# Kernel optimization log

Measured on AMD Instinct MI355X. Metric: run time of the kernel, lower is better.

## Reference

```python
import jax, jax.numpy as jnp
import numpy as np

T, B, H = 512, 256, 256


def setup_inputs() -> dict:
    key = jax.random.key(0)
    k1, k2, k3, k4 = jax.random.split(key, 4)
    ins = jax.random.normal(k1, (T, B, H), jnp.float32)
    resets = jax.random.randint(k2, (T, B), 0, 2) > 0  # bool reset mask
    carry = jnp.zeros((B, H), jnp.float32)
    scale = 1.0 / np.sqrt(H).astype(np.float32)
    # Fused GRU weights: columns ordered [r | z | n] for input and hidden projections.
    Wi = jax.random.normal(k3, (H, 3 * H), jnp.float32) * scale  # dense_i kernels (ir, iz, in)
    Wh = jax.random.normal(k4, (H, 3 * H), jnp.float32) * scale  # dense_h kernels (hr, hz, hn)
    bi = jnp.zeros((3 * H,), jnp.float32)   # dense_i biases (ir, iz, in)
    bhn = jnp.zeros((H,), jnp.float32)      # dense_h bias, only the 'hn' gate has one in flax GRUCell
    return dict(ins=ins, resets=resets, carry=carry, Wi=Wi, bi=bi, Wh=Wh, bhn=bhn)


def reference(ins, resets, carry, Wi, bi, Wh, bhn):
    """Faithful jax version of ScannedRNN: per-step reset-masked flax GRUCell scan.

    flax GRUCell math:
      r = sigmoid(x@Wir + bir + h@Whr)
      z = sigmoid(x@Wiz + biz + h@Whz)
      n = tanh(x@Win + bin + r * (h@Whn + bhn))
      h' = (1-z)*n + z*h ; output y = h'
    Reset mask zeroes the carry before the cell (initialize_carry -> zeros).
    """
    def step(h, xt):
        x, reset = xt  # x: [B,H], reset: [B]
        h = jnp.where(reset[:, None], jnp.zeros_like(h), h)
        gi = x @ Wi + bi          # [B, 3H]
        gh = h @ Wh               # [B, 3H]
        ir_, iz_, in_ = jnp.split(gi, 3, axis=-1)
        hr_, hz_, hn_ = jnp.split(gh, 3, axis=-1)
        r = jax.nn.sigmoid(ir_ + hr_)
        z = jax.nn.sigmoid(iz_ + hz_)
        n = jnp.tanh(in_ + r * (hn_ + bhn))
        h_new = (1.0 - z) * n + z * h
        return h_new, h_new

    _, ys = jax.lax.scan(step, carry, (ins, resets))
    return ys  # [T, B, H]
```

## Files before the change

kernel.cpp:

```cpp
#include <hip/hip_runtime.h>
#include <stdint.h>


typedef __attribute__((ext_vector_type(8))) __bf16 bf16x8;
typedef __attribute__((ext_vector_type(4))) float f32x4;

__device__ __forceinline__ float bf2f(unsigned short u) {
    union { unsigned int i; float f; } v; v.i = ((unsigned int)u) << 16; return v.f;
}
__device__ __forceinline__ unsigned short f2bf(float f) {
    union { float f; unsigned int i; } v; v.f = f;
    unsigned int x = v.i;
    x = x + 0x7fffu + ((x >> 16) & 1u);
    return (unsigned short)(x >> 16);
}
__device__ __forceinline__ float fsig(float x) {
    return __builtin_amdgcn_rcpf(1.f + __builtin_amdgcn_exp2f(-1.442695041f * x));
}
__device__ __forceinline__ float ftanh(float x) {
    return 1.f - 2.f * __builtin_amdgcn_rcpf(1.f + __builtin_amdgcn_exp2f(2.885390082f * x));
}

__global__ void prep_weights(const float* __restrict__ Wi, const float* __restrict__ Wh,
                             unsigned short* __restrict__ WiT, unsigned short* __restrict__ WhT) {
    const int idx = blockIdx.x * 256 + threadIdx.x;
    const float* src = blockIdx.y ? Wh : Wi;
    unsigned short* dst = blockIdx.y ? WhT : WiT;
    const int c = idx >> 8, k = idx & 255;
    dst[c * 256 + k] = f2bf(src[k * 768 + c]);
}

__launch_bounds__(512, 2)
__global__ void gi_gemm(const float* __restrict__ ins, const unsigned short* __restrict__ WiT,
                        const float* __restrict__ bi, unsigned int* __restrict__ GI32) {
    __shared__ unsigned short a_buf[2][16 * 264];

    const int tid = threadIdx.x;
    const int lane = tid & 63, wv = tid >> 6;
    const int quad = lane >> 4, n16 = lane & 15;

    bf16x8 wfrag[3][2][8];
#pragma unroll
    for (int g = 0; g < 3; ++g)
#pragma unroll
        for (int tl = 0; tl < 2; ++tl) {
            const int c = g * 256 + wv * 32 + tl * 16 + n16;
            const unsigned short* src = WiT + c * 256 + quad * 8;
#pragma unroll
            for (int kt = 0; kt < 8; ++kt)
                wfrag[g][tl][kt] = *(const bf16x8*)(src + kt * 32);
        }
    float bi_r[3][2];
#pragma unroll
    for (int g = 0; g < 3; ++g)
#pragma unroll
        for (int tl = 0; tl < 2; ++tl)
            bi_r[g][tl] = bi[g * 256 + wv * 32 + tl * 16 + n16];

    const int srow = tid >> 5;
    const int scol = (tid & 31) * 8;

    float4 p0, p1;
    {
        const float* p = ins + (size_t)blockIdx.x * 16 * 256 + tid * 8;
        p0 = *(const float4*)p; p1 = *(const float4*)(p + 4);
    }

    int buf = 0;
    for (int i = 0; i < 32; ++i) {
        const int chunk = blockIdx.x + i * 256;
        {
            bf16x8 av;
            av[0] = (__bf16)p0.x; av[1] = (__bf16)p0.y; av[2] = (__bf16)p0.z; av[3] = (__bf16)p0.w;
            av[4] = (__bf16)p1.x; av[5] = (__bf16)p1.y; av[6] = (__bf16)p1.z; av[7] = (__bf16)p1.w;
            *(bf16x8*)(&a_buf[buf][srow * 264 + scol]) = av;
        }
        if (i + 1 < 32) {
            const float* p = ins + (size_t)(blockIdx.x + (i + 1) * 256) * 16 * 256 + tid * 8;
            p0 = *(const float4*)p; p1 = *(const float4*)(p + 4);
        }
        __syncthreads();

        f32x4 acc[3][2] = {};
#pragma unroll
        for (int kt = 0; kt < 8; ++kt) {
            bf16x8 af = *(const bf16x8*)(&a_buf[buf][n16 * 264 + kt * 32 + quad * 8]);
#pragma unroll
            for (int g = 0; g < 3; ++g)
#pragma unroll
                for (int tl = 0; tl < 2; ++tl)
                    acc[g][tl] = __builtin_amdgcn_mfma_f32_16x16x32_bf16(af, wfrag[g][tl][kt], acc[g][tl], 0, 0, 0);
        }
        {
            const int t = chunk >> 4;
            const int b0 = (chunk & 15) * 16;
#pragma unroll
            for (int g = 0; g < 3; ++g)
#pragma unroll
                for (int r = 0; r < 4; ++r) {
                    const unsigned int lo = f2bf(acc[g][0][r] + bi_r[g][0]);
                    const unsigned int hi = f2bf(acc[g][1][r] + bi_r[g][1]);
                    GI32[((size_t)t * 256 + b0 + quad * 4 + r) * 384 + g * 128 + wv * 16 + n16] =
                        lo | (hi << 16);
                }
        }
        buf ^= 1;
    }
}

__launch_bounds__(512, 2)
__global__ void gru_scan(const unsigned short* __restrict__ GI, const int* __restrict__ resets,
                         const float* __restrict__ carry, const unsigned short* __restrict__ WhT,
                         const float* __restrict__ bhn, float* __restrict__ out) {
    __shared__ int s_reset[512];
    __shared__ unsigned short s_h[2][16 * 264];
    __shared__ unsigned int s_gi[2][16 * 386];
    const int b = blockIdx.x;
    const int tid = threadIdx.x;
    const int lane = tid & 63, wv = tid >> 6;
    const int quad = lane >> 4, n16 = lane & 15;

    s_reset[tid] = resets[tid * 256 + b];

    bf16x8 wfrag[3][2][8];
#pragma unroll
    for (int g = 0; g < 3; ++g)
#pragma unroll
        for (int tl = 0; tl < 2; ++tl) {
            const int c = g * 256 + wv * 32 + tl * 16 + n16;
            const unsigned short* src = WhT + c * 256 + quad * 8;
#pragma unroll
            for (int kt = 0; kt < 8; ++kt)
                wfrag[g][tl][kt] = *(const bf16x8*)(src + kt * 32);
        }
    float bhn_r[2];
    bhn_r[0] = bhn[wv * 32 + n16];
    bhn_r[1] = bhn[wv * 32 + 16 + n16];

    __syncthreads();

    int t_cur[4], t_end[4];
    float h_prev[2][4];
#pragma unroll
    for (int r = 0; r < 4; ++r) {
        const int slot = quad * 4 + r;
        const int w0 = slot * 32;
        int st = -1;
        for (int t = w0; t < w0 + 32; ++t)
            if (t == 0 || s_reset[t] != 0) { st = t; break; }
        int en = 511;
        for (int t = w0 + 32; t < 512; ++t)
            if (s_reset[t] != 0) { en = t - 1; break; }
        float h0 = 0.f, h1 = 0.f;
        if (st == 0 && s_reset[0] == 0) {
            h0 = carry[b * 256 + wv * 32 + n16];
            h1 = carry[b * 256 + wv * 32 + 16 + n16];
        }
        if (st < 0) { t_cur[r] = 1; t_end[r] = 0; }
        else        { t_cur[r] = st; t_end[r] = en; }
        h_prev[0][r] = h0; h_prev[1][r] = h1;
        s_h[0][slot * 264 + wv * 32 + n16] = f2bf(h0);
        s_h[0][slot * 264 + wv * 32 + 16 + n16] = f2bf(h1);
    }

    const int srcl = (wv >> 1) * 16;
    const unsigned short* gbase = GI + (size_t)b * 768;

    {
        int c0 = (t_cur[0] <= t_end[0]) ? t_cur[0] : 0;
        int c1 = (t_cur[1] <= t_end[1]) ? t_cur[1] : 0;
        int c2 = (t_cur[2] <= t_end[2]) ? t_cur[2] : 0;
        int c3 = (t_cur[3] <= t_end[3]) ? t_cur[3] : 0;
        const int v0 = __builtin_amdgcn_readlane(c0, srcl);
        const int v1 = __builtin_amdgcn_readlane(c1, srcl);
        const int v2 = __builtin_amdgcn_readlane(c2, srcl);
        const int v3 = __builtin_amdgcn_readlane(c3, srcl);
        const int r0 = (wv & 1) ? v2 : v0;
        const int r1 = (wv & 1) ? v3 : v1;
        const uint2* s0 = (const uint2*)(gbase + (size_t)r0 * 196608) + lane * 3;
        const uint2* s1 = (const uint2*)(gbase + (size_t)r1 * 196608) + lane * 3;
        uint2* d0 = (uint2*)(&s_gi[0][(2 * wv) * 386]) + lane * 3;
        uint2* d1 = (uint2*)(&s_gi[0][(2 * wv + 1) * 386]) + lane * 3;
        d0[0] = s0[0]; d0[1] = s0[1]; d0[2] = s0[2];
        d1[0] = s1[0]; d1[1] = s1[1]; d1[2] = s1[2];
    }
    __syncthreads();

    int buf = 0;
    for (int it = 0; it < 520; ++it) {
        const bool any = (t_cur[0] <= t_end[0]) | (t_cur[1] <= t_end[1]) |
                         (t_cur[2] <= t_end[2]) | (t_cur[3] <= t_end[3]);
        if (__ballot((int)any) == 0ull) break;

        uint2 pf0a, pf0b, pf0c, pf1a, pf1b, pf1c;
        {
            int s0_ = (t_cur[0] < t_end[0]) ? t_cur[0] + 1 : 0;
            int s1_ = (t_cur[1] < t_end[1]) ? t_cur[1] + 1 : 0;
            int s2_ = (t_cur[2] < t_end[2]) ? t_cur[2] + 1 : 0;
            int s3_ = (t_cur[3] < t_end[3]) ? t_cur[3] + 1 : 0;
            const int v0 = __builtin_amdgcn_readlane(s0_, srcl);
            const int v1 = __builtin_amdgcn_readlane(s1_, srcl);
            const int v2 = __builtin_amdgcn_readlane(s2_, srcl);
            const int v3 = __builtin_amdgcn_readlane(s3_, srcl);
            const int r0 = (wv & 1) ? v2 : v0;
            const int r1 = (wv & 1) ? v3 : v1;
            const uint2* s0 = (const uint2*)(gbase + (size_t)r0 * 196608) + lane * 3;
            const uint2* s1 = (const uint2*)(gbase + (size_t)r1 * 196608) + lane * 3;
            pf0a = s0[0]; pf0b = s0[1]; pf0c = s0[2];
            pf1a = s1[0]; pf1b = s1[1]; pf1c = s1[2];
        }

        f32x4 acc2[3][2] = {};
#pragma unroll
        for (int kt = 0; kt < 8; ++kt) {
            bf16x8 af = *(const bf16x8*)(&s_h[buf][n16 * 264 + kt * 32 + quad * 8]);
#pragma unroll
            for (int g = 0; g < 3; ++g)
#pragma unroll
                for (int tl = 0; tl < 2; ++tl)
                    acc2[g][tl] = __builtin_amdgcn_mfma_f32_16x16x32_bf16(af, wfrag[g][tl][kt], acc2[g][tl], 0, 0, 0);
        }

        float hn[2][4];
#pragma unroll
        for (int r = 0; r < 4; ++r) {
            const bool alive = t_cur[r] <= t_end[r];
            const unsigned int* gp = &s_gi[buf][(quad * 4 + r) * 386 + wv * 16 + n16];
            const unsigned int ur = gp[0], uz = gp[128], un = gp[256];
#pragma unroll
            for (int tl = 0; tl < 2; ++tl) {
                const int c = wv * 32 + tl * 16 + n16;
                const float gr = bf2f((unsigned short)(tl ? (ur >> 16) : (ur & 0xffffu)));
                const float gz = bf2f((unsigned short)(tl ? (uz >> 16) : (uz & 0xffffu)));
                const float gn = bf2f((unsigned short)(tl ? (un >> 16) : (un & 0xffffu)));
                const float rr = fsig(gr + acc2[0][tl][r]);
                const float zz = fsig(gz + acc2[1][tl][r]);
                const float nn = ftanh(gn + rr * (acc2[2][tl][r] + bhn_r[tl]));
                hn[tl][r] = (1.f - zz) * nn + zz * h_prev[tl][r];
                if (alive) out[((size_t)t_cur[r] * 256 + b) * 256 + c] = hn[tl][r];
            }
        }

#pragma unroll
        for (int r = 0; r < 4; ++r) {
            const int slot = quad * 4 + r;
            const bool alive = t_cur[r] <= t_end[r];
            const int tn = t_cur[r] + 1;
            const bool nalive = alive && (tn <= t_end[r]);
            float k0 = 0.f, k1 = 0.f;
            if (nalive && s_reset[tn & 511] == 0) { k0 = hn[0][r]; k1 = hn[1][r]; }
            h_prev[0][r] = k0; h_prev[1][r] = k1;
            s_h[buf ^ 1][slot * 264 + wv * 32 + n16] = f2bf(k0);
            s_h[buf ^ 1][slot * 264 + wv * 32 + 16 + n16] = f2bf(k1);
            if (alive) t_cur[r] = tn;
        }

        {
            uint2* d0 = (uint2*)(&s_gi[buf ^ 1][(2 * wv) * 386]) + lane * 3;
            uint2* d1 = (uint2*)(&s_gi[buf ^ 1][(2 * wv + 1) * 386]) + lane * 3;
            d0[0] = pf0a; d0[1] = pf0b; d0[2] = pf0c;
            d1[0] = pf1a; d1[1] = pf1b; d1[2] = pf1c;
        }
        __syncthreads();
        buf ^= 1;
    }
}

extern "C" void kernel_launch(void* const* d_in, const int* in_sizes, int n_in,
                              void* d_out, int out_size, void* d_ws, size_t ws_size,
                              hipStream_t stream) {
    const float* ins   = (const float*)d_in[0];
    const int* resets  = (const int*)d_in[1];
    const float* carry = (const float*)d_in[2];
    const float* Wi    = (const float*)d_in[3];
    const float* bi    = (const float*)d_in[4];
    const float* Wh    = (const float*)d_in[5];
    const float* bhn   = (const float*)d_in[6];
    float* out = (float*)d_out;

    unsigned short* WiT = (unsigned short*)d_ws;
    unsigned short* WhT = WiT + 196608;
    unsigned short* GI  = WhT + 196608;

    prep_weights<<<dim3(768, 2), dim3(256), 0, stream>>>(Wi, Wh, WiT, WhT);
    gi_gemm<<<dim3(256), dim3(512), 0, stream>>>(ins, WiT, bi, (unsigned int*)GI);
    gru_scan<<<dim3(256), dim3(512), 0, stream>>>(GI, resets, carry, WhT, bhn, out);
}
```

Baseline: 429.2 us.

## Move n-gate weights to swizzled LDS and read GI directly into registers

New measurement: 494.2 us. +15.2%, slower.

```diff
diff --git a/kernel.cpp b/kernel.cpp
--- a/kernel.cpp
+++ b/kernel.cpp
@@ -30,18 +30,31 @@
     dst[c * 256 + k] = f2bf(src[k * 768 + c]);
 }
 
+__device__ __forceinline__ void stage_wn(const unsigned short* __restrict__ WT,
+                                         unsigned short* __restrict__ s_wn, int tid) {
+#pragma unroll
+    for (int w = 0; w < 16; ++w) {
+        const int gi = tid + w * 512;
+        const int c = gi >> 5, gr = gi & 31;
+        bf16x8 v = *(const bf16x8*)(WT + (size_t)(512 + c) * 256 + gr * 8);
+        *(bf16x8*)(&s_wn[(c * 32 + (gr ^ (c & 7))) * 8]) = v;
+    }
+}
+
 __launch_bounds__(512, 2)
 __global__ void gi_gemm(const float* __restrict__ ins, const unsigned short* __restrict__ WiT,
                         const float* __restrict__ bi, unsigned int* __restrict__ GI32) {
-    __shared__ unsigned short a_buf[2][16 * 264];
+    __shared__ unsigned short s_wn[65536];
 
     const int tid = threadIdx.x;
     const int lane = tid & 63, wv = tid >> 6;
     const int quad = lane >> 4, n16 = lane & 15;
 
-    bf16x8 wfrag[3][2][8];
-#pragma unroll
-    for (int g = 0; g < 3; ++g)
+    stage_wn(WiT, s_wn, tid);
+
+    bf16x8 wfrag[2][2][8];
+#pragma unroll
+    for (int g = 0; g < 2; ++g)
 #pragma unroll
         for (int tl = 0; tl < 2; ++tl) {
             const int c = g * 256 + wv * 32 + tl * 16 + n16;
@@ -57,40 +70,41 @@
         for (int tl = 0; tl < 2; ++tl)
             bi_r[g][tl] = bi[g * 256 + wv * 32 + tl * 16 + n16];
 
-    const int srow = tid >> 5;
-    const int scol = (tid & 31) * 8;
-
-    float4 p0, p1;
-    {
-        const float* p = ins + (size_t)blockIdx.x * 16 * 256 + tid * 8;
-        p0 = *(const float4*)p; p1 = *(const float4*)(p + 4);
-    }
-
-    int buf = 0;
+    const int key = n16 & 7;
+    const int c0row = (wv * 32 + n16) * 32;
+    const int c1row = (wv * 32 + 16 + n16) * 32;
+
+    __syncthreads();
+
     for (int i = 0; i < 32; ++i) {
         const int chunk = blockIdx.x + i * 256;
-        {
-            bf16x8 av;
-            av[0] = (__bf16)p0.x; av[1] = (__bf16)p0.y; av[2] = (__bf16)p0.z; av[3] = (__bf16)p0.w;
-            av[4] = (__bf16)p1.x; av[5] = (__bf16)p1.y; av[6] = (__bf16)p1.z; av[7] = (__bf16)p1.w;
-            *(bf16x8*)(&a_buf[buf][srow * 264 + scol]) = av;
-        }
-        if (i + 1 < 32) {
-            const float* p = ins + (size_t)(blockIdx.x + (i + 1) * 256) * 16 * 256 + tid * 8;
-            p0 = *(const float4*)p; p1 = *(const float4*)(p + 4);
-        }
-        __syncthreads();
+        const float* arow = ins + ((size_t)chunk * 16 + n16) * 256 + quad * 8;
+        bf16x8 af[8];
+#pragma unroll
+        for (int kt = 0; kt < 8; ++kt) {
+            const float4 q0 = *(const float4*)(arow + kt * 32);
+            const float4 q1 = *(const float4*)(arow + kt * 32 + 4);
+            bf16x8 v;
+            v[0] = (__bf16)q0.x; v[1] = (__bf16)q0.y; v[2] = (__bf16)q0.z; v[3] = (__bf16)q0.w;
+            v[4] = (__bf16)q1.x; v[5] = (__bf16)q1.y; v[6] = (__bf16)q1.z; v[7] = (__bf16)q1.w;
+            af[kt] = v;
+        }
 
         f32x4 acc[3][2] = {};
 #pragma unroll
         for (int kt = 0; kt < 8; ++kt) {
-            bf16x8 af = *(const bf16x8*)(&a_buf[buf][n16 * 264 + kt * 32 + quad * 8]);
-#pragma unroll
-            for (int g = 0; g < 3; ++g)
+#pragma unroll
+            for (int g = 0; g < 2; ++g)
 #pragma unroll
                 for (int tl = 0; tl < 2; ++tl)
-                    acc[g][tl] = __builtin_amdgcn_mfma_f32_16x16x32_bf16(af, wfrag[g][tl][kt], acc[g][tl], 0, 0, 0);
-        }
+                    acc[g][tl] = __builtin_amdgcn_mfma_f32_16x16x32_bf16(af[kt], wfrag[g][tl][kt], acc[g][tl], 0, 0, 0);
+            const int gsw = ((kt * 4 + quad) ^ key) * 8;
+            const bf16x8 bn0 = *(const bf16x8*)(&s_wn[(c0row * 8) + gsw]);
+            const bf16x8 bn1 = *(const bf16x8*)(&s_wn[(c1row * 8) + gsw]);
+            acc[2][0] = __builtin_amdgcn_mfma_f32_16x16x32_bf16(af[kt], bn0, acc[2][0], 0, 0, 0);
+            acc[2][1] = __builtin_amdgcn_mfma_f32_16x16x32_bf16(af[kt], bn1, acc[2][1], 0, 0, 0);
+        }
+
         {
             const int t = chunk >> 4;
             const int b0 = (chunk & 15) * 16;
@@ -104,7 +118,6 @@
                         lo | (hi << 16);
                 }
         }
-        buf ^= 1;
     }
 }
 
@@ -114,17 +127,19 @@
                          const float* __restrict__ bhn, float* __restrict__ out) {
     __shared__ int s_reset[512];
     __shared__ unsigned short s_h[2][16 * 264];
-    __shared__ unsigned int s_gi[2][16 * 386];
+    __shared__ unsigned short s_wn[65536];
+
     const int b = blockIdx.x;
     const int tid = threadIdx.x;
     const int lane = tid & 63, wv = tid >> 6;
     const int quad = lane >> 4, n16 = lane & 15;
 
     s_reset[tid] = resets[tid * 256 + b];
-
-    bf16x8 wfrag[3][2][8];
-#pragma unroll
-    for (int g = 0; g < 3; ++g)
+    stage_wn(WhT, s_wn, tid);
+
+    bf16x8 wfrag[2][2][8];
+#pragma unroll
+    for (int g = 0; g < 2; ++g)
 #pragma unroll
         for (int tl = 0; tl < 2; ++tl) {
             const int c = g * 256 + wv * 32 + tl * 16 + n16;
@@ -136,6 +151,10 @@
     float bhn_r[2];
     bhn_r[0] = bhn[wv * 32 + n16];
     bhn_r[1] = bhn[wv * 32 + 16 + n16];
+
+    const int key = n16 & 7;
+    const int c0row = (wv * 32 + n16) * 32;
+    const int c1row = (wv * 32 + 16 + n16) * 32;
 
     __syncthreads();
 
@@ -163,107 +182,88 @@
         s_h[0][slot * 264 + wv * 32 + 16 + n16] = f2bf(h1);
     }
 
-    const int srcl = (wv >> 1) * 16;
-    const unsigned short* gbase = GI + (size_t)b * 768;
-
-    {
-        int c0 = (t_cur[0] <= t_end[0]) ? t_cur[0] : 0;
-        int c1 = (t_cur[1] <= t_end[1]) ? t_cur[1] : 0;
-        int c2 = (t_cur[2] <= t_end[2]) ? t_cur[2] : 0;
-        int c3 = (t_cur[3] <= t_end[3]) ? t_cur[3] : 0;
-        const int v0 = __builtin_amdgcn_readlane(c0, srcl);
-        const int v1 = __builtin_amdgcn_readlane(c1, srcl);
-        const int v2 = __builtin_amdgcn_readlane(c2, srcl);
-        const int v3 = __builtin_amdgcn_readlane(c3, srcl);
-        const int r0 = (wv & 1) ? v2 : v0;
-        const int r1 = (wv & 1) ? v3 : v1;
-        const uint2* s0 = (const uint2*)(gbase + (size_t)r0 * 196608) + lane * 3;
-        const uint2* s1 = (const uint2*)(gbase + (size_t)r1 * 196608) + lane * 3;
-        uint2* d0 = (uint2*)(&s_gi[0][(2 * wv) * 386]) + lane * 3;
-        uint2* d1 = (uint2*)(&s_gi[0][(2 * wv + 1) * 386]) + lane * 3;
-        d0[0] = s0[0]; d0[1] = s0[1]; d0[2] = s0[2];
-        d1[0] = s1[0]; d1[1] = s1[1]; d1[2] = s1[2];
-    }
+    const unsigned int* GI32b = (const unsigned int*)GI + (size_t)b * 384 + (wv * 16 + n16);
+    unsigned int gva[4][3], gvb[4][3];
+#pragma unroll
+    for (int r = 0; r < 4; ++r) {
+        const int tr0 = (t_cur[r] <= t_end[r]) ? t_cur[r] : 0;
+        const unsigned int* gp = GI32b + (size_t)tr0 * 98304;
+        gva[r][0] = gp[0]; gva[r][1] = gp[128]; gva[r][2] = gp[256];
+    }
+
     __syncthreads();
 
+#define SCAN_STEP(GCUR, GNXT)                                                                   \
+    {                                                                                           \
+        const bool any_ = (t_cur[0] <= t_end[0]) | (t_cur[1] <= t_end[1]) |                     \
+                          (t_cur[2] <= t_end[2]) | (t_cur[3] <= t_end[3]);                      \
+        if (__ballot((int)any_) == 0ull) break;                                                 \
+                                     \
+        _Pragma("unroll")                                                                       \
+        for (int r = 0; r < 4; ++r) {                                                           \
+            const int trn = (t_cur[r] < t_end[r]) ? (t_cur[r] + 1) : 0;                         \
+            const unsigned int* gp = GI32b + (size_t)trn * 98304;                               \
+            GNXT[r][0] = gp[0]; GNXT[r][1] = gp[128]; GNXT[r][2] = gp[256];                     \
+        }                                                                                       \
+                                                           \
+        f32x4 acc2[3][2] = {};                                                                  \
+        _Pragma("unroll")                                                                       \
+        for (int kt = 0; kt < 8; ++kt) {                                                        \
+            bf16x8 af = *(const bf16x8*)(&s_h[buf][n16 * 264 + kt * 32 + quad * 8]);            \
+            _Pragma("unroll")                                                                   \
+            for (int g = 0; g < 2; ++g)                                                         \
+                _Pragma("unroll")                                                               \
+                for (int tl = 0; tl < 2; ++tl)                                                  \
+                    acc2[g][tl] = __builtin_amdgcn_mfma_f32_16x16x32_bf16(af, wfrag[g][tl][kt], acc2[g][tl], 0, 0, 0); \
+            const int gsw = ((kt * 4 + quad) ^ key) * 8;                                        \
+            const bf16x8 bn0 = *(const bf16x8*)(&s_wn[(c0row * 8) + gsw]);                      \
+            const bf16x8 bn1 = *(const bf16x8*)(&s_wn[(c1row * 8) + gsw]);                      \
+            acc2[2][0] = __builtin_amdgcn_mfma_f32_16x16x32_bf16(af, bn0, acc2[2][0], 0, 0, 0); \
+            acc2[2][1] = __builtin_amdgcn_mfma_f32_16x16x32_bf16(af, bn1, acc2[2][1], 0, 0, 0); \
+        }                                                                                       \
+                                                              \
+        float hn[2][4];                                                                         \
+        _Pragma("unroll")                                                                       \
+        for (int r = 0; r < 4; ++r) {                                                           \
+            const bool alive = t_cur[r] <= t_end[r];                                            \
+            const unsigned int ur = GCUR[r][0], uz = GCUR[r][1], un = GCUR[r][2];               \
+            _Pragma("unroll")                                                                   \
+            for (int tl = 0; tl < 2; ++tl) {                                                    \
+                const int c = wv * 32 + tl * 16 + n16;                                          \
+                const float gr = bf2f((unsigned short)(tl ? (ur >> 16) : (ur & 0xffffu)));      \
+                const float gz = bf2f((unsigned short)(tl ? (uz >> 16) : (uz & 0xffffu)));      \
+                const float gn = bf2f((unsigned short)(tl ? (un >> 16) : (un & 0xffffu)));      \
+                const float rr = fsig(gr + acc2[0][tl][r]);                                     \
+                const float zz = fsig(gz + acc2[1][tl][r]);                                     \
+                const float nn = ftanh(gn + rr * (acc2[2][tl][r] + bhn_r[tl]));                 \
+                hn[tl][r] = (1.f - zz) * nn + zz * h_prev[tl][r];                               \
+                if (alive) out[((size_t)t_cur[r] * 256 + b) * 256 + c] = hn[tl][r];             \
+            }                                                                                   \
+        }                                                                                       \
+                                                   \
+        _Pragma("unroll")                                                                       \
+        for (int r = 0; r < 4; ++r) {                                                           \
+            const int slot = quad * 4 + r;                                                      \
+            const bool alive = t_cur[r] <= t_end[r];                                            \
+            const int tn = t_cur[r] + 1;                                                        \
+            const bool nalive = alive && (tn <= t_end[r]);                                      \
+            float k0 = 0.f, k1 = 0.f;                                                           \
+            if (nalive && s_reset[tn & 511] == 0) { k0 = hn[0][r]; k1 = hn[1][r]; }             \
+            h_prev[0][r] = k0; h_prev[1][r] = k1;                                               \
+            s_h[buf ^ 1][slot * 264 + wv * 32 + n16] = f2bf(k0);                                \
+            s_h[buf ^ 1][slot * 264 + wv * 32 + 16 + n16] = f2bf(k1);                           \
+            if (alive) t_cur[r] = tn;                                                           \
+        }                                                                                       \
+        __syncthreads();                           \
+        buf ^= 1;                                                                               \
+    }
+
     int buf = 0;
-    for (int it = 0; it < 520; ++it) {
-        const bool any = (t_cur[0] <= t_end[0]) | (t_cur[1] <= t_end[1]) |
-                         (t_cur[2] <= t_end[2]) | (t_cur[3] <= t_end[3]);
-        if (__ballot((int)any) == 0ull) break;
-
-        uint2 pf0a, pf0b, pf0c, pf1a, pf1b, pf1c;
-        {
-            int s0_ = (t_cur[0] < t_end[0]) ? t_cur[0] + 1 : 0;
-            int s1_ = (t_cur[1] < t_end[1]) ? t_cur[1] + 1 : 0;
-            int s2_ = (t_cur[2] < t_end[2]) ? t_cur[2] + 1 : 0;
-            int s3_ = (t_cur[3] < t_end[3]) ? t_cur[3] + 1 : 0;
-            const int v0 = __builtin_amdgcn_readlane(s0_, srcl);
-            const int v1 = __builtin_amdgcn_readlane(s1_, srcl);
-            const int v2 = __builtin_amdgcn_readlane(s2_, srcl);
-            const int v3 = __builtin_amdgcn_readlane(s3_, srcl);
-            const int r0 = (wv & 1) ? v2 : v0;
-            const int r1 = (wv & 1) ? v3 : v1;
-            const uint2* s0 = (const uint2*)(gbase + (size_t)r0 * 196608) + lane * 3;
-            const uint2* s1 = (const uint2*)(gbase + (size_t)r1 * 196608) + lane * 3;
-            pf0a = s0[0]; pf0b = s0[1]; pf0c = s0[2];
-            pf1a = s1[0]; pf1b = s1[1]; pf1c = s1[2];
-        }
-
-        f32x4 acc2[3][2] = {};
-#pragma unroll
-        for (int kt = 0; kt < 8; ++kt) {
-            bf16x8 af = *(const bf16x8*)(&s_h[buf][n16 * 264 + kt * 32 + quad * 8]);
-#pragma unroll
-            for (int g = 0; g < 3; ++g)
-#pragma unroll
-                for (int tl = 0; tl < 2; ++tl)
-                    acc2[g][tl] = __builtin_amdgcn_mfma_f32_16x16x32_bf16(af, wfrag[g][tl][kt], acc2[g][tl], 0, 0, 0);
-        }
-
-        float hn[2][4];
-#pragma unroll
-        for (int r = 0; r < 4; ++r) {
-            const bool alive = t_cur[r] <= t_end[r];
-            const unsigned int* gp = &s_gi[buf][(quad * 4 + r) * 386 + wv * 16 + n16];
-            const unsigned int ur = gp[0], uz = gp[128], un = gp[256];
-#pragma unroll
-            for (int tl = 0; tl < 2; ++tl) {
-                const int c = wv * 32 + tl * 16 + n16;
-                const float gr = bf2f((unsigned short)(tl ? (ur >> 16) : (ur & 0xffffu)));
-                const float gz = bf2f((unsigned short)(tl ? (uz >> 16) : (uz & 0xffffu)));
-                const float gn = bf2f((unsigned short)(tl ? (un >> 16) : (un & 0xffffu)));
-                const float rr = fsig(gr + acc2[0][tl][r]);
-                const float zz = fsig(gz + acc2[1][tl][r]);
-                const float nn = ftanh(gn + rr * (acc2[2][tl][r] + bhn_r[tl]));
-                hn[tl][r] = (1.f - zz) * nn + zz * h_prev[tl][r];
-                if (alive) out[((size_t)t_cur[r] * 256 + b) * 256 + c] = hn[tl][r];
-            }
-        }
-
-#pragma unroll
-        for (int r = 0; r < 4; ++r) {
-            const int slot = quad * 4 + r;
-            const bool alive = t_cur[r] <= t_end[r];
-            const int tn = t_cur[r] + 1;
-            const bool nalive = alive && (tn <= t_end[r]);
-            float k0 = 0.f, k1 = 0.f;
-            if (nalive && s_reset[tn & 511] == 0) { k0 = hn[0][r]; k1 = hn[1][r]; }
-            h_prev[0][r] = k0; h_prev[1][r] = k1;
-            s_h[buf ^ 1][slot * 264 + wv * 32 + n16] = f2bf(k0);
-            s_h[buf ^ 1][slot * 264 + wv * 32 + 16 + n16] = f2bf(k1);
-            if (alive) t_cur[r] = tn;
-        }
-
-        {
-            uint2* d0 = (uint2*)(&s_gi[buf ^ 1][(2 * wv) * 386]) + lane * 3;
-            uint2* d1 = (uint2*)(&s_gi[buf ^ 1][(2 * wv + 1) * 386]) + lane * 3;
-            d0[0] = pf0a; d0[1] = pf0b; d0[2] = pf0c;
-            d1[0] = pf1a; d1[1] = pf1b; d1[2] = pf1c;
-        }
-        __syncthreads();
-        buf ^= 1;
-    }
+    for (int it2 = 0; it2 < 260; ++it2) {
+        SCAN_STEP(gva, gvb)
+        SCAN_STEP(gvb, gva)
+    }
+#undef SCAN_STEP
 }
 
 extern "C" void kernel_launch(void* const* d_in, const int* in_sizes, int n_in,
```
